# Performance work log

Measured on AMD Instinct MI355X. Metric: run time of the kernel, lower is better.

The kernel has to match this reference:

```python
import jax, jax.numpy as jnp
import numpy as np

N = 100000   # nodes
E = 3200000  # edges
HIGH, LOW, EMB, HID, OUT = 384, 64, 128, 128, 2

def setup_inputs() -> dict:
    key = jax.random.key(0)
    ks = jax.random.split(key, 12)
    def lin(k, fan_in, fan_out):
        bound = 1.0 / np.sqrt(fan_in)
        kw, kb = jax.random.split(k)
        W = jax.random.uniform(kw, (fan_in, fan_out), jnp.float32, -bound, bound)
        b = jax.random.uniform(kb, (fan_out,), jnp.float32, -bound, bound)
        return W, b
    W_emb, b_emb = lin(ks[0], LOW, EMB)
    W1, b1 = lin(ks[1], HIGH + EMB, HID)
    W2, b2 = lin(ks[2], HID, HID)
    W_lin, b_lin = lin(ks[3], HID, OUT)
    return {
        "high_dim_features": jax.random.normal(ks[4], (N, HIGH), jnp.float32),
        "low_dim_features": jax.random.normal(ks[5], (N, LOW), jnp.float32),
        "edge_index": jax.random.randint(ks[6], (2, E), 0, N, jnp.int32),
        "W_emb": W_emb, "b_emb": b_emb,
        "W1": W1, "b1": b1,
        "W2": W2, "b2": b2,
        "W_lin": W_lin, "b_lin": b_lin,
    }

def _gcn_conv(x, W, b, src, dst, dis):
    # GCNConv: add self-loops, symmetric normalization D^-1/2 (A+I) D^-1/2
    xl = x @ W                                   # [N, out]
    norm = dis[src] * dis[dst]                   # [E]
    agg = jax.ops.segment_sum(xl[src] * norm[:, None], dst, num_segments=N)
    agg = agg + xl * (dis * dis)[:, None]        # self-loop term
    return agg + b

def reference(high_dim_features, low_dim_features, edge_index,
              W_emb, b_emb, W1, b1, W2, b2, W_lin, b_lin):
    src, dst = edge_index[0], edge_index[1]
    # degree with self-loops, computed on destination nodes (PyG default)
    deg = jax.ops.segment_sum(jnp.ones((E,), jnp.float32), dst, num_segments=N) + 1.0
    dis = jax.lax.rsqrt(deg)                     # deg >= 1 always

    low_emb = jax.nn.relu(low_dim_features @ W_emb + b_emb)
    x = jnp.concatenate([high_dim_features, low_emb], axis=1)  # [N, HIGH+EMB]
    x = jax.nn.relu(_gcn_conv(x, W1, b1, src, dst, dis))
    # dropout is identity in eval mode
    x = jax.nn.relu(_gcn_conv(x, W2, b2, src, dst, dis))
    x = x @ W_lin + b_lin
    return jax.nn.log_softmax(x, axis=1)
```

## Files before the change

kernel.cpp:

```cpp
#include <hip/hip_runtime.h>

#define HIGH 384
#define LOWD 64
#define EMB  128
#define HID  128

#define BINSHIFT 8
#define SRCBITS  17
#define SRCMASK  0x1FFFF
#define NBLK     256

typedef unsigned int u32;
typedef unsigned short u16;
typedef unsigned char u8;
typedef __attribute__((ext_vector_type(8))) short bf16x8;
typedef __attribute__((ext_vector_type(4))) float f32x4;
typedef __attribute__((ext_vector_type(2))) float f32x2;

__device__ __forceinline__ u32 pack_bf16(float a, float b) {
    u32 ua = __builtin_bit_cast(u32, a);
    u32 ub = __builtin_bit_cast(u32, b);
    ua += 0x7fffu + ((ua >> 16) & 1u);
    ub += 0x7fffu + ((ub >> 16) & 1u);
    return (ua >> 16) | (ub & 0xffff0000u);
}
__device__ __forceinline__ u16 pack1_bf16(float a) {
    u32 ua = __builtin_bit_cast(u32, a);
    ua += 0x7fffu + ((ua >> 16) & 1u);
    return (u16)(ua >> 16);
}
__device__ __forceinline__ u8 pack1_fp8(float a) {
    int r = __builtin_amdgcn_cvt_pk_fp8_f32(a, a, 0, false);
    return (u8)(r & 0xff);
}


__global__ void k_dis(const int* __restrict__ cnt, float* __restrict__ dis, int N) {
    int i = blockIdx.x * 256 + threadIdx.x;
    if (i < N) dis[i] = rsqrtf((float)cnt[i] + 1.0f);
}

__global__ void k_castw_all(const float* __restrict__ W1, u16* __restrict__ Wt1,
                            const float* __restrict__ W2, u16* __restrict__ Wt2,
                            const float* __restrict__ WE, u16* __restrict__ WtE) {
    int i = blockIdx.x * 256 + threadIdx.x;
    if (i < 65536) {
        int k = i >> 7, c = i & 127;
        Wt1[c * 512 + k] = pack1_bf16(W1[i]);
    } else if (i < 81920) {
        int j = i - 65536;
        int k = j >> 7, c = j & 127;
        Wt2[c * 128 + k] = pack1_bf16(W2[j]);
    } else if (i < 90112) {
        int j = i - 81920;
        int k = j >> 7, c = j & 127;
        WtE[c * 64 + k] = pack1_bf16(WE[j]);
    }
}


__global__ __launch_bounds__(256) void k_binhist(const int* __restrict__ dst, int E,
                                                 int* __restrict__ cnts, int NB) {
    __shared__ int hist[512];
    for (int b = threadIdx.x; b < NB; b += 256) hist[b] = 0;
    __syncthreads();
    int CH = (E + gridDim.x - 1) / gridDim.x;
    int e0 = blockIdx.x * CH;
    int e1 = min(E, e0 + CH);
    for (int e = e0 + threadIdx.x; e < e1; e += 256)
        atomicAdd(&hist[dst[e] >> BINSHIFT], 1);
    __syncthreads();
    for (int b = threadIdx.x; b < NB; b += 256)
        cnts[b * NBLK + blockIdx.x] = hist[b];
}

__global__ __launch_bounds__(256) void k_binscatter(const int* __restrict__ src,
                                                    const int* __restrict__ dst, int E,
                                                    const int* __restrict__ cnts,
                                                    u32* __restrict__ packed, int NB) {
    __shared__ int cur[512];
    for (int b = threadIdx.x; b < NB; b += 256) cur[b] = cnts[b * NBLK + blockIdx.x];
    __syncthreads();
    int CH = (E + gridDim.x - 1) / gridDim.x;
    int e0 = blockIdx.x * CH;
    int e1 = min(E, e0 + CH);
    for (int e = e0 + threadIdx.x; e < e1; e += 256) {
        int d = dst[e];
        int s = src[e];
        int bin = d >> BINSHIFT;
        int pos = atomicAdd(&cur[bin], 1);
        packed[pos] = (u32)s | ((u32)(d & 255) << SRCBITS);
    }
}

__global__ __launch_bounds__(256) void k_hist2(const u32* __restrict__ packed,
                                               const int* __restrict__ cnts, int E,
                                               int* __restrict__ cnt, int NB, int N) {
    __shared__ int hist[256];
    int t = threadIdx.x;
    hist[t] = 0;
    __syncthreads();
    int b = blockIdx.x;
    int begin = cnts[b * NBLK];
    int end = (b + 1 < NB) ? cnts[(b + 1) * NBLK] : E;
    for (int e = begin + t; e < end; e += 256)
        atomicAdd(&hist[packed[e] >> SRCBITS], 1);
    __syncthreads();
    int idx = (b << BINSHIFT) + t;
    if (idx < N) cnt[idx] = hist[t];
}

__global__ __launch_bounds__(256) void k_fill2(const u32* __restrict__ packed,
                                               const int* __restrict__ cnts, int E,
                                               const int* __restrict__ row_start,
                                               int* __restrict__ csr, int NB, int N) {
    __shared__ int cur[256];
    int t = threadIdx.x;
    int b = blockIdx.x;
    int base = b << BINSHIFT;
    cur[t] = row_start[min(base + t, N)];
    __syncthreads();
    int begin = cnts[b * NBLK];
    int end = (b + 1 < NB) ? cnts[(b + 1) * NBLK] : E;
    for (int e = begin + t; e < end; e += 256) {
        u32 p = packed[e];
        int pos = atomicAdd(&cur[p >> SRCBITS], 1);
        csr[pos] = (int)((p & SRCMASK) << 5);
    }
}


__global__ void k_scan1(const int* __restrict__ in, int n, int* __restrict__ bsums) {
    __shared__ int sh[256];
    int t = threadIdx.x;
    int base = blockIdx.x * 1024 + t * 4;
    int s = 0;
#pragma unroll
    for (int j = 0; j < 4; j++) { int idx = base + j; s += (idx < n) ? in[idx] : 0; }
    sh[t] = s; __syncthreads();
    for (int off = 128; off > 0; off >>= 1) {
        if (t < off) sh[t] += sh[t + off];
        __syncthreads();
    }
    if (t == 0) bsums[blockIdx.x] = sh[0];
}

__global__ void k_scan2(int* bsums, int nb) {
    if (threadIdx.x == 0 && blockIdx.x == 0) {
        int run = 0;
        for (int i = 0; i < nb; i++) { int v = bsums[i]; bsums[i] = run; run += v; }
    }
}

__global__ void k_scan3_flat(int* __restrict__ data, int n, const int* __restrict__ bsums) {
    __shared__ int sh[256];
    int t = threadIdx.x;
    int base = blockIdx.x * 1024 + t * 4;
    int v[4]; int s = 0;
#pragma unroll
    for (int j = 0; j < 4; j++) { int idx = base + j; v[j] = (idx < n) ? data[idx] : 0; s += v[j]; }
    sh[t] = s; __syncthreads();
    int x = s;
    for (int off = 1; off < 256; off <<= 1) {
        int y = (t >= off) ? sh[t - off] : 0;
        __syncthreads();
        x += y; sh[t] = x;
        __syncthreads();
    }
    int run = bsums[blockIdx.x] + (x - s);
#pragma unroll
    for (int j = 0; j < 4; j++) {
        int idx = base + j;
        if (idx < n) data[idx] = run;
        run += v[j];
    }
}

__global__ void k_scan3_rows(const int* __restrict__ cnt, int N, const int* __restrict__ bsums,
                             int* __restrict__ row_start, int E) {
    __shared__ int sh[256];
    int t = threadIdx.x;
    int base = blockIdx.x * 1024 + t * 4;
    int v[4]; int s = 0;
#pragma unroll
    for (int j = 0; j < 4; j++) { int idx = base + j; v[j] = (idx < N) ? cnt[idx] : 0; s += v[j]; }
    sh[t] = s; __syncthreads();
    int x = s;
    for (int off = 1; off < 256; off <<= 1) {
        int y = (t >= off) ? sh[t - off] : 0;
        __syncthreads();
        x += y; sh[t] = x;
        __syncthreads();
    }
    int run = bsums[blockIdx.x] + (x - s);
#pragma unroll
    for (int j = 0; j < 4; j++) {
        int idx = base + j;
        if (idx < N) row_start[idx] = run;
        run += v[j];
    }
    if (blockIdx.x == 0 && t == 0) row_start[N] = E;
}


template<bool A1BF, bool BIAS, bool RELU, bool SCALE, int OUT>
__global__ __launch_bounds__(256, 6) void k_mgemm(
    const void* __restrict__ A1v, int K1,
    const u32* __restrict__ A2, int K2,
    const u16* __restrict__ Wt,
    const float* __restrict__ bias,
    const float* __restrict__ dis,
    void* __restrict__ Cv, int M)
{
    __shared__ u32 Als[2][64][16];
    __shared__ u32 Bls[2][128][16];

    const int tid = threadIdx.x;
    const int l = tid & 63;
    const int w = tid >> 6;
    const int g = l >> 4;
    const int lr = l & 15;
    const int blockRow = blockIdx.x * 64;
    const int K = K1 + K2;
    const int T = K >> 5;

    const int ar = tid >> 2;
    const int ak = tid & 3;
    int arow = blockRow + ar; if (arow >= M) arow = M - 1;
    const int awb = (ak + ((ar >> 1) & 3)) & 3;

    const int wc = tid >> 1;
    const int wh = tid & 1;
    const int wsw = (wc >> 1) & 3;
    const int wb0 = (wh * 2 + wsw) & 3;
    const int wb1 = (wh * 2 + 1 + wsw) & 3;

    const float* a1f = (const float*)A1v + (size_t)arow * K1;
    const u32*   a1b = (const u32*)A1v + (size_t)arow * (K1 >> 1);
    const u32*   a2b = A2 + (size_t)arow * (K2 >> 1);
    const u32*   wtb = (const u32*)Wt + (size_t)wc * (K >> 1);

    f32x4 acc[8];
#pragma unroll
    for (int j = 0; j < 8; j++) acc[j] = (f32x4)0.f;

    u32 pa[4], wk[8];

    auto load_tile = [&](int k0) {
        if (k0 < K1) {
            if (A1BF) {
                uint4 a = *(const uint4*)(a1b + (k0 >> 1) + ak * 4);
                pa[0] = a.x; pa[1] = a.y; pa[2] = a.z; pa[3] = a.w;
            } else {
                const float* src = a1f + k0 + ak * 8;
                float4 f0 = *(const float4*)(src + 0);
                float4 f1 = *(const float4*)(src + 4);
                pa[0] = pack_bf16(f0.x, f0.y); pa[1] = pack_bf16(f0.z, f0.w);
                pa[2] = pack_bf16(f1.x, f1.y); pa[3] = pack_bf16(f1.z, f1.w);
            }
        } else {
            uint4 a = *(const uint4*)(a2b + ((k0 - K1) >> 1) + ak * 4);
            pa[0] = a.x; pa[1] = a.y; pa[2] = a.z; pa[3] = a.w;
        }
        const u32* srcw = wtb + ((k0 + wh * 16) >> 1);
        uint4 a = *(const uint4*)srcw;
        uint4 b = *(const uint4*)(srcw + 4);
        wk[0] = a.x; wk[1] = a.y; wk[2] = a.z; wk[3] = a.w;
        wk[4] = b.x; wk[5] = b.y; wk[6] = b.z; wk[7] = b.w;
    };
    auto store_tile = [&](int buf) {
        *(uint4*)&Als[buf][ar][awb * 4] = make_uint4(pa[0], pa[1], pa[2], pa[3]);
        *(uint4*)&Bls[buf][wc][wb0 * 4] = make_uint4(wk[0], wk[1], wk[2], wk[3]);
        *(uint4*)&Bls[buf][wc][wb1 * 4] = make_uint4(wk[4], wk[5], wk[6], wk[7]);
    };

    load_tile(0);
    store_tile(0);
    __syncthreads();

    for (int t = 0; t < T; t++) {
        const int cur = t & 1;
        const bool more = (t + 1 < T);
        if (more) load_tile((t + 1) << 5);

        bf16x8 af;
        {
            int r = w * 16 + lr;
            int blk = (g + ((r >> 1) & 3)) & 3;
            af = *(const bf16x8*)&Als[cur][r][blk * 4];
        }
#pragma unroll
        for (int cb = 0; cb < 8; cb++) {
            int c = cb * 16 + lr;
            int blk = (g + ((c >> 1) & 3)) & 3;
            bf16x8 bf = *(const bf16x8*)&Bls[cur][c][blk * 4];
            acc[cb] = __builtin_amdgcn_mfma_f32_16x16x32_bf16(af, bf, acc[cb], 0, 0, 0);
        }
        if (more) store_tile(cur ^ 1);
        __syncthreads();
    }

    float disv[4];
    if (SCALE) {
#pragma unroll
        for (int j = 0; j < 4; j++) {
            int row = blockRow + w * 16 + g * 4 + j;
            disv[j] = (row < M) ? dis[row] : 0.f;
        }
    }
#pragma unroll
    for (int cb = 0; cb < 8; cb++) {
        int col = cb * 16 + lr;
        float bv = BIAS ? bias[col] : 0.f;
#pragma unroll
        for (int j = 0; j < 4; j++) {
            int row = blockRow + w * 16 + g * 4 + j;
            if (row < M) {
                float v = acc[cb][j];
                if (BIAS) v += bv;
                if (SCALE) v *= disv[j];
                if (RELU) v = fmaxf(v, 0.f);
                if (OUT == 0) {
                    ((u16*)Cv)[(size_t)row * 128 + col] = pack1_bf16(v);
                } else {
                    ((u8*)Cv)[(size_t)row * 128 + col] = pack1_fp8(v);
                }
            }
        }
    }
}


template<int MODE>
__global__ __launch_bounds__(256) void k_gatherw(
    const u32* __restrict__ xls32, const int* __restrict__ row_start,
    const int* __restrict__ csr, const float* __restrict__ dis,
    const float* __restrict__ bias, const float* __restrict__ Wl,
    const float* __restrict__ bl, void* __restrict__ outv, int N)
{
    int wave = threadIdx.x >> 6;
    int lane = threadIdx.x & 63;
    int half = lane >> 5;
    int w32 = lane & 31;
    int n = blockIdx.x * 4 + wave;
    if (n >= N) return;
    int jb = row_start[n], je = row_start[n + 1];

    float a0 = 0.f, a1 = 0.f, a2 = 0.f, a3 = 0.f;
    {
        u32 v = xls32[(u32)n * 32 + w32];
        if (half == 0) {
            f32x2 lo = __builtin_amdgcn_cvt_pk_f32_fp8((int)v, false);
            f32x2 hi = __builtin_amdgcn_cvt_pk_f32_fp8((int)v, true);
            a0 = lo.x; a1 = lo.y; a2 = hi.x; a3 = hi.y;
        }
    }

    int j = jb;
    for (; j + 7 < je; j += 8) {
        int c0 = csr[j + 4 * half + 0];
        int c1 = csr[j + 4 * half + 1];
        int c2 = csr[j + 4 * half + 2];
        int c3 = csr[j + 4 * half + 3];
        u32 v0 = xls32[(u32)c0 + w32];
        u32 v1 = xls32[(u32)c1 + w32];
        u32 v2 = xls32[(u32)c2 + w32];
        u32 v3 = xls32[(u32)c3 + w32];
        f32x2 l0 = __builtin_amdgcn_cvt_pk_f32_fp8((int)v0, false);
        f32x2 h0 = __builtin_amdgcn_cvt_pk_f32_fp8((int)v0, true);
        f32x2 l1 = __builtin_amdgcn_cvt_pk_f32_fp8((int)v1, false);
        f32x2 h1 = __builtin_amdgcn_cvt_pk_f32_fp8((int)v1, true);
        f32x2 l2 = __builtin_amdgcn_cvt_pk_f32_fp8((int)v2, false);
        f32x2 h2 = __builtin_amdgcn_cvt_pk_f32_fp8((int)v2, true);
        f32x2 l3 = __builtin_amdgcn_cvt_pk_f32_fp8((int)v3, false);
        f32x2 h3 = __builtin_amdgcn_cvt_pk_f32_fp8((int)v3, true);
        a0 += (l0.x + l1.x) + (l2.x + l3.x);
        a1 += (l0.y + l1.y) + (l2.y + l3.y);
        a2 += (h0.x + h1.x) + (h2.x + h3.x);
        a3 += (h0.y + h1.y) + (h2.y + h3.y);
    }
    for (; j + 3 < je; j += 4) {
        int c0 = csr[j + 2 * half];
        int c1 = csr[j + 2 * half + 1];
        u32 v0 = xls32[(u32)c0 + w32];
        u32 v1 = xls32[(u32)c1 + w32];
        f32x2 l0 = __builtin_amdgcn_cvt_pk_f32_fp8((int)v0, false);
        f32x2 h0 = __builtin_amdgcn_cvt_pk_f32_fp8((int)v0, true);
        f32x2 l1 = __builtin_amdgcn_cvt_pk_f32_fp8((int)v1, false);
        f32x2 h1 = __builtin_amdgcn_cvt_pk_f32_fp8((int)v1, true);
        a0 += l0.x + l1.x; a1 += l0.y + l1.y;
        a2 += h0.x + h1.x; a3 += h0.y + h1.y;
    }
    if (j + 1 < je) {
        int c = csr[j + half];
        u32 v = xls32[(u32)c + w32];
        f32x2 lo = __builtin_amdgcn_cvt_pk_f32_fp8((int)v, false);
        f32x2 hi = __builtin_amdgcn_cvt_pk_f32_fp8((int)v, true);
        a0 += lo.x; a1 += lo.y; a2 += hi.x; a3 += hi.y;
        j += 2;
    }
    if (j < je) {
        int c = csr[j];
        u32 v = xls32[(u32)c + w32];
        if (half == 0) {
            f32x2 lo = __builtin_amdgcn_cvt_pk_f32_fp8((int)v, false);
            f32x2 hi = __builtin_amdgcn_cvt_pk_f32_fp8((int)v, true);
            a0 += lo.x; a1 += lo.y; a2 += hi.x; a3 += hi.y;
        }
    }

    a0 += __shfl(a0, w32 + 32);
    a1 += __shfl(a1, w32 + 32);
    a2 += __shfl(a2, w32 + 32);
    a3 += __shfl(a3, w32 + 32);

    float d = dis[n];
    float4 bv = *(const float4*)&bias[w32 * 4];
    float h0v = fmaxf(fmaf(d, a0, bv.x), 0.f);
    float h1v = fmaxf(fmaf(d, a1, bv.y), 0.f);
    float h2v = fmaxf(fmaf(d, a2, bv.z), 0.f);
    float h3v = fmaxf(fmaf(d, a3, bv.w), 0.f);

    if (MODE == 0) {
        if (half == 0) {
            uint2 pw;
            pw.x = pack_bf16(h0v, h1v);
            pw.y = pack_bf16(h2v, h3v);
            *(uint2*)((u32*)outv + (size_t)n * 64 + w32 * 2) = pw;
        }
    } else {
        float4 q0 = *(const float4*)&Wl[w32 * 8];
        float4 q1 = *(const float4*)&Wl[w32 * 8 + 4];
        float p0 = h0v * q0.x + h1v * q0.z + h2v * q1.x + h3v * q1.z;
        float p1 = h0v * q0.y + h1v * q0.w + h2v * q1.y + h3v * q1.w;
#pragma unroll
        for (int off = 16; off > 0; off >>= 1) {
            p0 += __shfl_down(p0, off);
            p1 += __shfl_down(p1, off);
        }
        if (lane == 0) {
            float z0 = p0 + bl[0], z1 = p1 + bl[1];
            float m = fmaxf(z0, z1);
            float ls = m + logf(expf(z0 - m) + expf(z1 - m));
            float* out = (float*)outv;
            out[(size_t)n * 2 + 0] = z0 - ls;
            out[(size_t)n * 2 + 1] = z1 - ls;
        }
    }
}


extern "C" void kernel_launch(void* const* d_in, const int* in_sizes, int n_in,
                              void* d_out, int out_size, void* d_ws, size_t ws_size,
                              hipStream_t stream) {
    const float* high  = (const float*)d_in[0];
    const float* low   = (const float*)d_in[1];
    const int*   ei    = (const int*)d_in[2];
    const float* W_emb = (const float*)d_in[3];
    const float* b_emb = (const float*)d_in[4];
    const float* W1    = (const float*)d_in[5];
    const float* b1    = (const float*)d_in[6];
    const float* W2    = (const float*)d_in[7];
    const float* b2    = (const float*)d_in[8];
    const float* Wl    = (const float*)d_in[9];
    const float* bl    = (const float*)d_in[10];

    int N = in_sizes[0] / HIGH;
    int E = in_sizes[2] / 2;
    const int* srcp = ei;
    const int* dstp = ei + E;
    float* out = (float*)d_out;

    int NB = (N + 255) >> BINSHIFT;
    int NSCAN = NB * NBLK;

    char* ws = (char*)d_ws;
    size_t off = 0;
    auto alloc = [&](size_t b) { size_t o = off; off += (b + 255) & ~(size_t)255; return o; };
    float* dis       = (float*)(ws + alloc((size_t)N * 4));
    int*   cnt       = (int*)  (ws + alloc((size_t)N * 4));
    int*   row_start = (int*)  (ws + alloc((size_t)(N + 1) * 4));
    int*   bsums     = (int*)  (ws + alloc(4096));
    int*   cnts      = (int*)  (ws + alloc((size_t)NSCAN * 4));
    u32*   packed    = (u32*)  (ws + alloc((size_t)E * 4));
    int*   csr       = (int*)  (ws + alloc((size_t)E * 4));
    u16*   Wt1       = (u16*)  (ws + alloc((size_t)512 * 128 * 2));
    u16*   Wt2       = (u16*)  (ws + alloc((size_t)128 * 128 * 2));
    u16*   WtE       = (u16*)  (ws + alloc((size_t)64 * 128 * 2));
    u16*   bufE      = (u16*)  (ws + alloc((size_t)N * 128 * 2));
    u8*    bufX      = (u8*)   (ws + alloc((size_t)N * 128));
    u16*   bufH      = (u16*)  (ws + alloc((size_t)N * 128 * 2));
    (void)ws_size; (void)n_in; (void)out_size;

    int nbS = (NSCAN + 1023) / 1024;
    int nbN = (N + 1023) / 1024;
    int mt  = (N + 63) / 64;

    k_castw_all<<<(90112 + 255) / 256, 256, 0, stream>>>(W1, Wt1, W2, Wt2, W_emb, WtE);

    k_binhist<<<NBLK, 256, 0, stream>>>(dstp, E, cnts, NB);
    k_scan1<<<nbS, 256, 0, stream>>>(cnts, NSCAN, bsums);
    k_scan2<<<1, 64, 0, stream>>>(bsums, nbS);
    k_scan3_flat<<<nbS, 256, 0, stream>>>(cnts, NSCAN, bsums);
    k_binscatter<<<NBLK, 256, 0, stream>>>(srcp, dstp, E, cnts, packed, NB);
    k_hist2<<<NB, 256, 0, stream>>>(packed, cnts, E, cnt, NB, N);
    k_dis<<<(N + 255) / 256, 256, 0, stream>>>(cnt, dis, N);
    k_scan1<<<nbN, 256, 0, stream>>>(cnt, N, bsums);
    k_scan2<<<1, 64, 0, stream>>>(bsums, nbN);
    k_scan3_rows<<<nbN, 256, 0, stream>>>(cnt, N, bsums, row_start, E);
    k_fill2<<<NB, 256, 0, stream>>>(packed, cnts, E, row_start, csr, NB, N);

    k_mgemm<false, true, true, false, 0><<<mt, 256, 0, stream>>>(
        low, LOWD, (const u32*)bufE, 0, WtE, b_emb, nullptr, bufE, N);
    k_mgemm<false, false, false, true, 1><<<mt, 256, 0, stream>>>(
        high, HIGH, (const u32*)bufE, EMB, Wt1, nullptr, dis, bufX, N);
    k_gatherw<0><<<(N + 3) / 4, 256, 0, stream>>>(
        (const u32*)bufX, row_start, csr, dis, b1, nullptr, nullptr, bufH, N);
    k_mgemm<true, false, false, true, 1><<<mt, 256, 0, stream>>>(
        bufH, HID, (const u32*)bufH, 0, Wt2, nullptr, dis, bufX, N);
    k_gatherw<1><<<(N + 3) / 4, 256, 0, stream>>>(
        (const u32*)bufX, row_start, csr, dis, b2, Wl, bl, out, N);
}
```

Baseline: 371.8 us.

## Replace LDS-staged GEMM with direct global-to-register MFMA fragment loads

The dense GEMMs no longer stage A and W tiles through shared memory with barriers. Each lane now loads its MFMA fragments straight from global memory into registers, double-buffered across two k-steps, and K dimensions become template constants. This removes LDS traffic and __syncthreads, but every wave now reloads the full weight matrix from global/L2 and register pressure rises (occupancy hint lowered from 6 to 4).

```diff
diff --git a/kernel.cpp b/kernel.cpp
--- a/kernel.cpp
+++ b/kernel.cpp
@@ -203,17 +203,18 @@
 }
 
 
-template<bool A1BF, bool BIAS, bool RELU, bool SCALE, int OUT>
-__global__ __launch_bounds__(256, 6) void k_mgemm(
-    const void* __restrict__ A1v, int K1,
-    const u32* __restrict__ A2, int K2,
+template<int K1, int K2, bool A1BF, bool BIAS, bool RELU, bool SCALE, int OUT>
+__global__ __launch_bounds__(256, 4) void k_dgemm(
+    const void* __restrict__ A1v,
+    const u16* __restrict__ A2h,
     const u16* __restrict__ Wt,
     const float* __restrict__ bias,
     const float* __restrict__ dis,
     void* __restrict__ Cv, int M)
 {
-    __shared__ u32 Als[2][64][16];
-    __shared__ u32 Bls[2][128][16];
+    constexpr int K = K1 + K2;
+    constexpr int T = K >> 5;
+    static_assert((T & 1) == 0, "T must be even");
 
     const int tid = threadIdx.x;
     const int l = tid & 63;
@@ -221,83 +222,54 @@
     const int g = l >> 4;
     const int lr = l & 15;
     const int blockRow = blockIdx.x * 64;
-    const int K = K1 + K2;
-    const int T = K >> 5;
-
-    const int ar = tid >> 2;
-    const int ak = tid & 3;
-    int arow = blockRow + ar; if (arow >= M) arow = M - 1;
-    const int awb = (ak + ((ar >> 1) & 3)) & 3;
-
-    const int wc = tid >> 1;
-    const int wh = tid & 1;
-    const int wsw = (wc >> 1) & 3;
-    const int wb0 = (wh * 2 + wsw) & 3;
-    const int wb1 = (wh * 2 + 1 + wsw) & 3;
+
+    int arow = blockRow + w * 16 + lr;
+    if (arow >= M) arow = M - 1;
 
     const float* a1f = (const float*)A1v + (size_t)arow * K1;
-    const u32*   a1b = (const u32*)A1v + (size_t)arow * (K1 >> 1);
-    const u32*   a2b = A2 + (size_t)arow * (K2 >> 1);
-    const u32*   wtb = (const u32*)Wt + (size_t)wc * (K >> 1);
+    const u16*   a1h = (const u16*)A1v + (size_t)arow * K1;
+    const u16*   a2h = A2h + (size_t)arow * K2;
+    const u16*   wt0 = Wt + (size_t)lr * K + g * 8;
 
     f32x4 acc[8];
 #pragma unroll
     for (int j = 0; j < 8; j++) acc[j] = (f32x4)0.f;
 
-    u32 pa[4], wk[8];
-
-    auto load_tile = [&](int k0) {
-        if (k0 < K1) {
+    auto load_frags = [&](int t, bf16x8& af, bf16x8* bf) {
+        const int k0 = t * 32;
+        if (K2 == 0 || k0 < K1) {
             if (A1BF) {
-                uint4 a = *(const uint4*)(a1b + (k0 >> 1) + ak * 4);
-                pa[0] = a.x; pa[1] = a.y; pa[2] = a.z; pa[3] = a.w;
+                af = *(const bf16x8*)(a1h + k0 + g * 8);
             } else {
-                const float* src = a1f + k0 + ak * 8;
-                float4 f0 = *(const float4*)(src + 0);
-                float4 f1 = *(const float4*)(src + 4);
-                pa[0] = pack_bf16(f0.x, f0.y); pa[1] = pack_bf16(f0.z, f0.w);
-                pa[2] = pack_bf16(f1.x, f1.y); pa[3] = pack_bf16(f1.z, f1.w);
+                const float* s = a1f + k0 + g * 8;
+                float4 f0 = *(const float4*)s;
+                float4 f1 = *(const float4*)(s + 4);
+                uint4 u = make_uint4(pack_bf16(f0.x, f0.y), pack_bf16(f0.z, f0.w),
+                                     pack_bf16(f1.x, f1.y), pack_bf16(f1.z, f1.w));
+                af = __builtin_bit_cast(bf16x8, u);
             }
         } else {
-            uint4 a = *(const uint4*)(a2b + ((k0 - K1) >> 1) + ak * 4);
-            pa[0] = a.x; pa[1] = a.y; pa[2] = a.z; pa[3] = a.w;
-        }
-        const u32* srcw = wtb + ((k0 + wh * 16) >> 1);
-        uint4 a = *(const uint4*)srcw;
-        uint4 b = *(const uint4*)(srcw + 4);
-        wk[0] = a.x; wk[1] = a.y; wk[2] = a.z; wk[3] = a.w;
-        wk[4] = b.x; wk[5] = b.y; wk[6] = b.z; wk[7] = b.w;
+            af = *(const bf16x8*)(a2h + (k0 - K1) + g * 8);
+        }
+#pragma unroll
+        for (int cb = 0; cb < 8; cb++)
+            bf[cb] = *(const bf16x8*)(wt0 + (size_t)cb * 16 * K + k0);
     };
-    auto store_tile = [&](int buf) {
-        *(uint4*)&Als[buf][ar][awb * 4] = make_uint4(pa[0], pa[1], pa[2], pa[3]);
-        *(uint4*)&Bls[buf][wc][wb0 * 4] = make_uint4(wk[0], wk[1], wk[2], wk[3]);
-        *(uint4*)&Bls[buf][wc][wb1 * 4] = make_uint4(wk[4], wk[5], wk[6], wk[7]);
+    auto do_mfma = [&](bf16x8 af, bf16x8* bf) {
+#pragma unroll
+        for (int cb = 0; cb < 8; cb++)
+            acc[cb] = __builtin_amdgcn_mfma_f32_16x16x32_bf16(af, bf[cb], acc[cb], 0, 0, 0);
     };
 
-    load_tile(0);
-    store_tile(0);
-    __syncthreads();
-
-    for (int t = 0; t < T; t++) {
-        const int cur = t & 1;
-        const bool more = (t + 1 < T);
-        if (more) load_tile((t + 1) << 5);
-
-        bf16x8 af;
-        {
-            int r = w * 16 + lr;
-            int blk = (g + ((r >> 1) & 3)) & 3;
-            af = *(const bf16x8*)&Als[cur][r][blk * 4];
-        }
-#pragma unroll
-        for (int cb = 0; cb < 8; cb++) {
-            int c = cb * 16 + lr;
-            int blk = (g + ((c >> 1) & 3)) & 3;
-            bf16x8 bf = *(const bf16x8*)&Bls[cur][c][blk * 4];
-            acc[cb] = __builtin_amdgcn_mfma_f32_16x16x32_bf16(af, bf, acc[cb], 0, 0, 0);
-        }
-        if (more) store_tile(cur ^ 1);
-        __syncthreads();
+    bf16x8 aA, aB;
+    bf16x8 bA[8], bB[8];
+    load_frags(0, aA, bA);
+#pragma unroll 1
+    for (int t = 0; t < T; t += 2) {
+        load_frags(t + 1, aB, bB);
+        do_mfma(aA, bA);
+        if (t + 2 < T) load_frags(t + 2, aA, bA);
+        do_mfma(aB, bB);
     }
 
     float disv[4];
@@ -510,14 +482,14 @@
     k_scan3_rows<<<nbN, 256, 0, stream>>>(cnt, N, bsums, row_start, E);
     k_fill2<<<NB, 256, 0, stream>>>(packed, cnts, E, row_start, csr, NB, N);
 
-    k_mgemm<false, true, true, false, 0><<<mt, 256, 0, stream>>>(
-        low, LOWD, (const u32*)bufE, 0, WtE, b_emb, nullptr, bufE, N);
-    k_mgemm<false, false, false, true, 1><<<mt, 256, 0, stream>>>(
-        high, HIGH, (const u32*)bufE, EMB, Wt1, nullptr, dis, bufX, N);
+    k_dgemm<LOWD, 0, false, true, true, false, 0><<<mt, 256, 0, stream>>>(
+        low, nullptr, WtE, b_emb, nullptr, bufE, N);
+    k_dgemm<HIGH, EMB, false, false, false, true, 1><<<mt, 256, 0, stream>>>(
+        high, bufE, Wt1, nullptr, dis, bufX, N);
     k_gatherw<0><<<(N + 3) / 4, 256, 0, stream>>>(
         (const u32*)bufX, row_start, csr, dis, b1, nullptr, nullptr, bufH, N);
-    k_mgemm<true, false, false, true, 1><<<mt, 256, 0, stream>>>(
-        bufH, HID, (const u32*)bufH, 0, Wt2, nullptr, dis, bufX, N);
+    k_dgemm<HID, 0, true, false, false, true, 1><<<mt, 256, 0, stream>>>(
+        bufH, nullptr, Wt2, nullptr, dis, bufX, N);
     k_gatherw<1><<<(N + 3) / 4, 256, 0, stream>>>(
         (const u32*)bufX, row_start, csr, dis, b2, Wl, bl, out, N);
 }
```

Result: slower. 473.4 us (+27.3%).
